# Optimization experiments

Hardware: AMD Instinct MI355X
Metric: run time of the kernel (lower is better)

Reference implementation:

```python
import jax, jax.numpy as jnp
import numpy as np

B, P, C = 8, 16384, 5          # images, proposals/img, classes (incl. background)
K = 100                         # detections_per_img (greedy-NMS iterations)
SCORE_THRESH = 0.05
NMS_THRESH = 0.5
W_XY, W_WH = 10.0, 5.0          # bbox_reg_weights (10,10,5,5)
BBOX_XFORM_CLIP = float(np.log(1000.0 / 16.0))
NEG = jnp.float32(-1e30)


def setup_inputs() -> dict:
    key = jax.random.key(0)
    ks = jax.random.split(key, 8)
    N = B * P
    class_logits = jax.random.normal(ks[0], (N, C), jnp.float32)
    box_regression = jax.random.normal(ks[1], (N, C * 4), jnp.float32) * 0.1
    handside_logits = jax.random.normal(ks[2], (N, C), jnp.float32)
    dxdymag_logits = jax.random.normal(ks[3], (N, C * 3), jnp.float32)
    contact_logits = jax.random.normal(ks[4], (N, C * 5), jnp.float32)
    # valid proposal boxes x1<x2, y1<y2 inside an ~800x1216 image
    x1 = jax.random.uniform(ks[5], (B, P), jnp.float32) * 1100.0
    y1 = jax.random.uniform(ks[6], (B, P), jnp.float32) * 700.0
    wh = jax.random.uniform(ks[7], (B, P, 2), jnp.float32) * 100.0 + 4.0
    proposals = jnp.stack([x1, y1, x1 + wh[..., 0], y1 + wh[..., 1]], axis=-1)
    image_hw = jnp.array([800, 1216], jnp.int32)
    return dict(class_logits=class_logits, box_regression=box_regression,
                handside_logits=handside_logits, dxdymag_logits=dxdymag_logits,
                contact_logits=contact_logits, proposals=proposals, image_hw=image_hw)


def _decode(rel, props):
    # rel [N,C,4], props [N,4] -> [N,C,4] (torchvision BoxCoder.decode)
    w = props[:, 2] - props[:, 0]
    h = props[:, 3] - props[:, 1]
    cx = props[:, 0] + 0.5 * w
    cy = props[:, 1] + 0.5 * h
    dx = rel[..., 0] / W_XY
    dy = rel[..., 1] / W_XY
    dw = jnp.minimum(rel[..., 2] / W_WH, BBOX_XFORM_CLIP)
    dh = jnp.minimum(rel[..., 3] / W_WH, BBOX_XFORM_CLIP)
    pcx = dx * w[:, None] + cx[:, None]
    pcy = dy * h[:, None] + cy[:, None]
    pw = jnp.exp(dw) * w[:, None]
    ph = jnp.exp(dh) * h[:, None]
    return jnp.stack([pcx - 0.5 * pw, pcy - 0.5 * ph,
                      pcx + 0.5 * pw, pcy + 0.5 * ph], axis=-1)


def _iou_one_vs_all(box, boxes):
    lt = jnp.maximum(box[:2], boxes[:, :2])
    rb = jnp.minimum(box[2:], boxes[:, 2:])
    whd = jnp.clip(rb - lt, 0.0)
    inter = whd[:, 0] * whd[:, 1]
    a1 = (box[2] - box[0]) * (box[3] - box[1])
    a2 = (boxes[:, 2] - boxes[:, 0]) * (boxes[:, 3] - boxes[:, 1])
    return inter / (a1 + a2 - inter)


def _nms_image(boxes, scores, labels):
    # class-aware greedy NMS (batched_nms coordinate-offset trick), fixed K iters.
    off = labels.astype(boxes.dtype) * (jax.lax.stop_gradient(boxes).max() + 1.0)
    obox = jax.lax.stop_gradient(boxes) + off[:, None]

    def step(s, _):
        i = jnp.argmax(s)
        keep = s[i] > NEG * 0.5
        iou = _iou_one_vs_all(obox[i], obox)
        s = jnp.where((iou > NMS_THRESH) & keep, NEG, s)
        s = s.at[i].set(NEG)
        return s, (i, keep)

    _, (idx, keep) = jax.lax.scan(step, scores, None, length=K)
    return idx, keep


def reference(class_logits, box_regression, handside_logits, dxdymag_logits,
              contact_logits, proposals, image_hw):
    N = class_logits.shape[0]
    pred_boxes = _decode(box_regression.reshape(N, C, 4), proposals.reshape(-1, 4))
    pred_scores = jax.nn.softmax(class_logits, axis=-1)          # [N,C]
    pred_sides = (jax.nn.sigmoid(handside_logits) > 0.5).astype(jnp.float32)
    pred_dxdy = dxdymag_logits.reshape(N, C, 3)
    pred_contacts = jnp.argmax(contact_logits.reshape(N, C, 5), axis=2)
    # clip boxes to image (image_shape = (H, W))
    Hh = image_hw[0].astype(jnp.float32)
    Ww = image_hw[1].astype(jnp.float32)
    xs = jnp.clip(pred_boxes[..., 0::2], 0.0, Ww)
    ys = jnp.clip(pred_boxes[..., 1::2], 0.0, Hh)
    pred_boxes = jnp.stack([xs[..., 0], ys[..., 0], xs[..., 1], ys[..., 1]], -1)
    # drop background class, flatten per image (class-fastest order, as torch reshape)
    Cm1 = C - 1
    boxes = pred_boxes[:, 1:].reshape(B, P * Cm1, 4)
    scores = pred_scores[:, 1:].reshape(B, P * Cm1)
    sides = pred_sides[:, 1:].reshape(B, P * Cm1)
    dxdy = pred_dxdy[:, 1:].reshape(B, P * Cm1, 3)
    contacts = pred_contacts[:, 1:].reshape(B, P * Cm1)
    labels = jnp.broadcast_to(jnp.tile(jnp.arange(1, C), P), (B, P * Cm1))
    # score thresholding via masking (scores <= thresh never selected)
    ms = jnp.where(scores > SCORE_THRESH, scores, NEG)
    idx, keep = jax.vmap(_nms_image)(boxes, ms, labels)          # [B,K]
    kf = keep.astype(jnp.float32)
    out_boxes = jnp.take_along_axis(boxes, idx[:, :, None], 1) * kf[:, :, None]
    out_scores = jnp.take_along_axis(scores, idx, 1) * kf
    out_labels = jnp.where(keep, jnp.take_along_axis(labels, idx, 1), 0)
    out_sides = jnp.take_along_axis(sides, idx, 1) * kf
    out_dxdy = jnp.take_along_axis(dxdy, idx[:, :, None], 1) * kf[:, :, None]
    out_contacts = jnp.where(keep, jnp.take_along_axis(contacts, idx, 1), 0)
    return (out_boxes, out_scores, out_labels, out_sides, out_dxdy, out_contacts, keep)
```

## Files before the change

### kernel.cpp

```cpp
#include <hip/hip_runtime.h>
#include <cstdint>

typedef unsigned int u32;
typedef unsigned long long u64;

constexpr int B_ = 8;
constexpr int P_ = 16384;
constexpr int K_ = 100;
constexpr int M_ = P_ * 4;
constexpr int TSEL = 192;
constexpr int CAP = 256;
constexpr int NBP = 576;
constexpr u32 BASE16 = 0x3D4Cu;
constexpr float SCORE_T = 0.05f;
constexpr float CLIPV = 4.135166556742356f;


__device__ inline int aphys(int i) {
  return (i < CAP) ? ((((i & 63) + ((i >> 6) << 2)) & 63) | (i & 192)) : i;
}

__device__ inline float4 decode_clip(float4 rel, float4 pr, float Wf, float Hf) {
  const float w  = pr.z - pr.x;
  const float h  = pr.w - pr.y;
  const float cx = pr.x + 0.5f * w;
  const float cy = pr.y + 0.5f * h;
  const float dx = rel.x / 10.0f;
  const float dy = rel.y / 10.0f;
  const float dw = fminf(rel.z / 5.0f, CLIPV);
  const float dh = fminf(rel.w / 5.0f, CLIPV);
  const float pcx = dx * w + cx;
  const float pcy = dy * h + cy;
  const float pw = expf(dw) * w;
  const float ph = expf(dh) * h;
  float x1 = pcx - 0.5f * pw, y1 = pcy - 0.5f * ph;
  float x2 = pcx + 0.5f * pw, y2 = pcy + 0.5f * ph;
  x1 = fminf(fmaxf(x1, 0.f), Wf);
  x2 = fminf(fmaxf(x2, 0.f), Wf);
  y1 = fminf(fmaxf(y1, 0.f), Hf);
  y2 = fminf(fmaxf(y2, 0.f), Hf);
  return make_float4(x1, y1, x2, y2);
}

__global__ __launch_bounds__(256) void prep_kernel(
    const float* __restrict__ logits, const float* __restrict__ boxreg,
    const float* __restrict__ props, const int* __restrict__ image_hw,
    float* __restrict__ wscores, float* __restrict__ wblockmax,
    u32* __restrict__ bhist)
{
  __shared__ u32 lh[NBP];
  __shared__ float red[256];
  for (int i = threadIdx.x; i < NBP; i += 256) lh[i] = 0u;
  __syncthreads();

  const int n = blockIdx.x * 256 + threadIdx.x;

  float l[5];
#pragma unroll
  for (int i = 0; i < 5; ++i) l[i] = logits[n * 5 + i];
  float mx = l[0];
#pragma unroll
  for (int i = 1; i < 5; ++i) mx = fmaxf(mx, l[i]);
  float e[5]; float ssum = 0.f;
#pragma unroll
  for (int i = 0; i < 5; ++i) { e[i] = expf(l[i] - mx); ssum += e[i]; }

  const float4 pr = reinterpret_cast<const float4*>(props)[n];
  const float Hf = (float)image_hw[0];
  const float Wf = (float)image_hw[1];

  float bmax = 0.f;
  float sc[4];
#pragma unroll
  for (int c = 1; c < 5; ++c) {
    const float4 rel = reinterpret_cast<const float4*>(boxreg)[n * 5 + c];
    const float4 bx = decode_clip(rel, pr, Wf, Hf);
    bmax = fmaxf(bmax, fmaxf(fmaxf(bx.x, bx.z), fmaxf(bx.y, bx.w)));
    const float sv = e[c] / ssum;
    sc[c - 1] = sv;
    if (sv > SCORE_T) {
      u32 bin = (__float_as_uint(sv) >> 16) - BASE16;
      if (bin >= (u32)NBP) bin = NBP - 1;
      atomicAdd(&lh[bin], 1u);
    }
  }
  reinterpret_cast<float4*>(wscores)[n] = make_float4(sc[0], sc[1], sc[2], sc[3]);

  __syncthreads();
  for (int i = threadIdx.x; i < NBP; i += 256)
    bhist[(size_t)blockIdx.x * NBP + i] = lh[i];

  red[threadIdx.x] = bmax;
  __syncthreads();
#pragma unroll
  for (int off = 128; off > 0; off >>= 1) {
    if (threadIdx.x < off) red[threadIdx.x] = fmaxf(red[threadIdx.x], red[threadIdx.x + off]);
    __syncthreads();
  }
  if (threadIdx.x == 0) wblockmax[blockIdx.x] = red[0];
}

__global__ __launch_bounds__(64) void thresh_kernel(
    const u32* __restrict__ bhist, u32* __restrict__ Xthr, int* __restrict__ Carr,
    int* __restrict__ remv, int* __restrict__ offs)
{
  const int b = blockIdx.x, t = threadIdx.x;
  const u32* base = bhist + (size_t)(b * 64) * NBP;
  const int lo = NBP - t * 9 - 9;

  u32 hb[9] = {0, 0, 0, 0, 0, 0, 0, 0, 0};
  for (int g = 0; g < 64; ++g) {
    const u32* hg = base + g * NBP + lo;
#pragma unroll
    for (int q = 0; q < 9; ++q) hb[q] += hg[q];
  }
  int mysum = 0;
#pragma unroll
  for (int q = 0; q < 9; ++q) mysum += (int)hb[q];

  int inc = mysum;
#pragma unroll
  for (int off = 1; off < 64; off <<= 1) {
    const int v = __shfl_up(inc, off);
    if (t >= off) inc += v;
  }
  const int tot = __shfl(inc, 63);
  const int pre = inc - mysum;

  int Xi = 0, Cv = 0, remV = 0, binXv = 0;
  if (tot < TSEL) {
    if (t == 63) { Xi = (int)(BASE16 << 16); Cv = tot; remV = 0; binXv = 0; }
  } else if (pre < TSEL && inc >= TSEL) {
    int cum = pre, kb = lo, qsel = 8;
    for (int q = 8; q >= 0; --q) {
      cum += (int)hb[q];
      if (cum >= TSEL) { kb = lo + q; qsel = q; break; }
    }
    int C = cum;
    int Xbin;
    if (C > CAP) { C -= (int)hb[qsel]; Xbin = kb + 1; }
    else Xbin = kb;
    Xi = (int)((BASE16 + (u32)Xbin) << 16);
    Cv = C; remV = tot - C; binXv = Xbin;
  }
#pragma unroll
  for (int off = 32; off > 0; off >>= 1) {
    Xi    = max(Xi,    __shfl_xor(Xi, off));
    Cv    = max(Cv,    __shfl_xor(Cv, off));
    remV  = max(remV,  __shfl_xor(remV, off));
    binXv = max(binXv, __shfl_xor(binXv, off));
  }

  int cg = 0;
  {
    const u32* hg = base + (size_t)t * NBP;
    for (int bin = binXv; bin < NBP; ++bin) cg += (int)hg[bin];
  }
  int inc2 = cg;
#pragma unroll
  for (int off = 1; off < 64; off <<= 1) {
    const int v = __shfl_up(inc2, off);
    if (t >= off) inc2 += v;
  }
  offs[b * 64 + t] = inc2 - cg;
  if (t == 0) { Xthr[b] = (u32)Xi; Carr[b] = Cv; remv[b] = remV; }
}

__global__ __launch_bounds__(256) void compact_kernel(
    const float* __restrict__ wscores, const u32* __restrict__ Xthr,
    const int* __restrict__ offs, u64* __restrict__ keybuf)
{
  const int blk = blockIdx.x;
  const int b = blk >> 6;
  const int n = blk * 256 + threadIdx.x;
  const u32 X = Xthr[b];
  __shared__ int cnt;
  if (threadIdx.x == 0) cnt = 0;
  __syncthreads();
  const int base = b * CAP + offs[blk];

  const float4 v = reinterpret_cast<const float4*>(wscores)[n];
  const float ss[4] = {v.x, v.y, v.z, v.w};
  const int j0 = (n & (P_ - 1)) * 4;
#pragma unroll
  for (int c = 0; c < 4; ++c) {
    if (ss[c] > SCORE_T) {
      const u32 bb = __float_as_uint(ss[c]);
      if (bb >= X) {
        const int pos = atomicAdd(&cnt, 1);
        keybuf[base + pos] = ((u64)bb << 16) | (u64)(65535 - (j0 + c));
      }
    }
  }
}

__global__ __launch_bounds__(512) void nms_kernel(
    const float* __restrict__ boxreg, const float* __restrict__ props,
    const int* __restrict__ image_hw,
    const float* __restrict__ wscores, const float* __restrict__ wblockmax,
    const u32* __restrict__ Xthr, const int* __restrict__ remv,
    const int* __restrict__ Carr, const u64* __restrict__ keybuf,
    const float* __restrict__ handside, const float* __restrict__ dxdymag,
    const float* __restrict__ contact, float* __restrict__ out)
{
  const int b = blockIdx.x, t = threadIdx.x;
  const float4* sc4 = reinterpret_cast<const float4*>(wscores) + (size_t)b * (M_ / 4);
  const u32 X = Xthr[b];
  const float Hf = (float)image_hw[0];
  const float Wf = (float)image_hw[1];

  __shared__ float maxv_s;
  __shared__ u64   kall[CAP];
  __shared__ u64   skey[CAP];
  __shared__ float4 cb4[CAP + K_];
  __shared__ float4 cbx[CAP + K_];
  __shared__ float carea[CAP + K_];
  __shared__ float cscf[CAP + K_];
  __shared__ int   cj[CAP + K_];
  __shared__ u64   supmask[CAP * 4];
  __shared__ int   kidx[K_];
  __shared__ int   kcount_s, nslow_s;
  __shared__ u64   red2[512];
  __shared__ u64   bitmap[1024];

  if (t < 64) {
    float v = wblockmax[b * 64 + t];
#pragma unroll
    for (int off = 32; off > 0; off >>= 1) v = fmaxf(v, __shfl_xor(v, off));
    if (t == 0) maxv_s = v;
  }
  if (t == 0) { kcount_s = 0; nslow_s = 0; }
  const int C = min(Carr[b], CAP);
  if (t < CAP) kall[t] = (t < C) ? keybuf[b * CAP + t] : 0ull;
  __syncthreads();
  const float maxv1 = maxv_s + 1.0f;

  if (t < CAP) {
    const u64 my = kall[t];
    u32 r = 0;
    for (int u = 0; u < CAP; ++u) r += (kall[u] > my) ? 1u : 0u;
    if (t < C) skey[r] = my;
  }
  __syncthreads();

  if (t < C) {
    const u64 key = skey[t];
    const int j = 65535 - (int)(key & 0xFFFFull);
    const int cls = (j & 3) + 1;
    const int n = b * P_ + (j >> 2);
    const float4 rel = reinterpret_cast<const float4*>(boxreg)[n * 5 + cls];
    const float4 pr  = reinterpret_cast<const float4*>(props)[n];
    const float4 bx = decode_clip(rel, pr, Wf, Hf);
    const float offv = (float)cls * maxv1;
    const float ox1 = bx.x + offv, oy1 = bx.y + offv;
    const float ox2 = bx.z + offv, oy2 = bx.w + offv;
    const int ph = aphys(t);
    cb4[ph] = make_float4(ox1, oy1, ox2, oy2);
    cbx[ph] = bx;
    carea[ph] = (ox2 - ox1) * (oy2 - oy1);
    cscf[ph] = __uint_as_float((u32)(key >> 16));
    cj[ph] = j;
  }
  __syncthreads();

  for (int task = t; task < C * 4; task += 512) {
    const int i = task >> 2, wq = task & 3;
    const float4 ib = cb4[aphys(i)];
    const float ia = carea[aphys(i)];
    u64 m = 0;
    const int qb = wq * 64, qe = min(qb + 64, C);
    for (int q = qb; q < qe; ++q) {
      if (q == i) continue;
      const int qp = aphys(q);
      const float4 qbx = cb4[qp];
      const float ltx = fmaxf(ib.x, qbx.x);
      const float lty = fmaxf(ib.y, qbx.y);
      const float rbx = fminf(ib.z, qbx.z);
      const float rby = fminf(ib.w, qbx.w);
      const float iw = fmaxf(rbx - ltx, 0.f);
      const float ih = fmaxf(rby - lty, 0.f);
      const float inter = iw * ih;
      const float iou = inter / (ia + carea[qp] - inter);
      if (iou > 0.5f) m |= 1ull << (q - qb);
    }
    supmask[i * 4 + wq] = m;
  }
  __syncthreads();

  if (t < 64) {
    const u64 lowm = t ? (~0ull >> (64 - t)) : 0ull;
    u64 rb[4][4];
    bool alv[4];
#pragma unroll
    for (int q = 0; q < 4; ++q) {
      const int r = q * 64 + t;
      alv[q] = (r < C);
#pragma unroll
      for (int w = 0; w < 4; ++w) {
        u64 m = supmask[r * 4 + w];
        if (w == q) m &= lowm;
        else if (w > q) m = 0ull;
        rb[q][w] = m;
      }
    }
    u64 km0 = __ballot(alv[0]);
    u64 km1 = __ballot(alv[1]);
    u64 km2 = __ballot(alv[2]);
    u64 km3 = __ballot(alv[3]);
    for (int round = 0; round <= CAP; ++round) {
      const bool k0 = alv[0] && !((rb[0][0] & km0) | (rb[0][1] & km1) | (rb[0][2] & km2) | (rb[0][3] & km3));
      const bool k1 = alv[1] && !((rb[1][0] & km0) | (rb[1][1] & km1) | (rb[1][2] & km2) | (rb[1][3] & km3));
      const bool k2 = alv[2] && !((rb[2][0] & km0) | (rb[2][1] & km1) | (rb[2][2] & km2) | (rb[2][3] & km3));
      const bool k3 = alv[3] && !((rb[3][0] & km0) | (rb[3][1] & km1) | (rb[3][2] & km2) | (rb[3][3] & km3));
      const u64 n0 = __ballot(k0);
      const u64 n1 = __ballot(k1);
      const u64 n2 = __ballot(k2);
      const u64 n3 = __ballot(k3);
      if (n0 == km0 && n1 == km1 && n2 == km2 && n3 == km3) break;
      km0 = n0; km1 = n1; km2 = n2; km3 = n3;
    }
#pragma unroll
    for (int q = 0; q < 4; ++q) {
      const u64 kmq = (q == 0) ? km0 : (q == 1) ? km1 : (q == 2) ? km2 : km3;
      if ((kmq >> t) & 1ull) {
        int rank = __popcll(kmq & lowm);
        if (q > 0) rank += __popcll(km0);
        if (q > 1) rank += __popcll(km1);
        if (q > 2) rank += __popcll(km2);
        if (rank < K_) kidx[rank] = q * 64 + t;
      }
    }
    if (t == 0) {
      kcount_s = min(__popcll(km0) + __popcll(km1) +
                     __popcll(km2) + __popcll(km3), K_);
    }
  }
  __syncthreads();

  if (kcount_s < K_ && remv[b] > 0) {
    for (int i = t; i < 1024; i += 512) bitmap[i] = 0ull;
    __syncthreads();
    while (true) {
      u64 best = 0ull;
      for (int i = t; i < M_ / 4; i += 512) {
        const float4 v = sc4[i];
        const float ss[4] = {v.x, v.y, v.z, v.w};
#pragma unroll
        for (int c = 0; c < 4; ++c) {
          if (ss[c] > SCORE_T) {
            const u32 bb = __float_as_uint(ss[c]);
            if (bb < X) {
              const int j = i * 4 + c;
              if (!((bitmap[j >> 6] >> (j & 63)) & 1ull)) {
                const u64 key = ((u64)bb << 16) | (u64)(65535 - j);
                if (key > best) best = key;
              }
            }
          }
        }
      }
      red2[t] = best;
      __syncthreads();
      for (int off = 256; off > 0; off >>= 1) {
        if (t < off && red2[t + off] > red2[t]) red2[t] = red2[t + off];
        __syncthreads();
      }
      const u64 wkey = red2[0];
      if (wkey == 0ull) break;
      if (t == 0) {
        const int j = 65535 - (int)(wkey & 0xFFFFull);
        bitmap[j >> 6] |= 1ull << (j & 63);
        const int cls = (j & 3) + 1;
        const int n = b * P_ + (j >> 2);
        const float4 rel = reinterpret_cast<const float4*>(boxreg)[n * 5 + cls];
        const float4 pr  = reinterpret_cast<const float4*>(props)[n];
        const float4 bx = decode_clip(rel, pr, Wf, Hf);
        const float offv = (float)cls * maxv1;
        const float ox1 = bx.x + offv, oy1 = bx.y + offv;
        const float ox2 = bx.z + offv, oy2 = bx.w + offv;
        const float ar = (ox2 - ox1) * (oy2 - oy1);
        bool sup = false;
        for (int k2 = 0; k2 < kcount_s; ++k2) {
          const int ki = aphys(kidx[k2]);
          const float4 kb = cb4[ki];
          const float ltx = fmaxf(kb.x, ox1);
          const float lty = fmaxf(kb.y, oy1);
          const float rbx = fminf(kb.z, ox2);
          const float rby = fminf(kb.w, oy2);
          const float iw = fmaxf(rbx - ltx, 0.f);
          const float ih = fmaxf(rby - lty, 0.f);
          const float inter = iw * ih;
          const float iou = inter / (carea[ki] + ar - inter);
          if (iou > 0.5f) { sup = true; break; }
        }
        if (!sup) {
          const int slot = CAP + nslow_s;
          cb4[slot] = make_float4(ox1, oy1, ox2, oy2);
          cbx[slot] = bx;
          carea[slot] = ar;
          cscf[slot] = __uint_as_float((u32)(wkey >> 16));
          cj[slot] = j;
          kidx[kcount_s] = slot;
          ++nslow_s;
          ++kcount_s;
        }
      }
      __syncthreads();
      if (kcount_s >= K_) break;
    }
    __syncthreads();
  }
  __syncthreads();

  const int kc = kcount_s;
  if (t < K_) {
    const int r = t;
    float ob0 = 0.f, ob1 = 0.f, ob2 = 0.f, ob3 = 0.f;
    float osc = 0.f, olab = 0.f, oside = 0.f;
    float od0 = 0.f, od1 = 0.f, od2 = 0.f;
    float ocon = 0.f, okeep = 0.f;
    if (r < kc) {
      const int idx = kidx[r];
      const int ph = aphys(idx);
      const int j = cj[ph];
      const int cls = (j & 3) + 1;
      const int n = b * P_ + (j >> 2);
      const float4 bx = cbx[ph];
      ob0 = bx.x; ob1 = bx.y; ob2 = bx.z; ob3 = bx.w;
      osc = cscf[ph];
      olab = (float)cls;
      oside = (handside[n * 5 + cls] > 0.f) ? 1.f : 0.f;
      od0 = dxdymag[n * 15 + cls * 3 + 0];
      od1 = dxdymag[n * 15 + cls * 3 + 1];
      od2 = dxdymag[n * 15 + cls * 3 + 2];
      float bvv = contact[n * 25 + cls * 5 + 0];
      int best = 0;
#pragma unroll
      for (int i = 1; i < 5; ++i) {
        const float ci = contact[n * 25 + cls * 5 + i];
        if (ci > bvv) { bvv = ci; best = i; }
      }
      ocon = (float)best;
      okeep = 1.f;
    }
    const int gb = b * K_ + r;
    out[gb * 4 + 0] = ob0;
    out[gb * 4 + 1] = ob1;
    out[gb * 4 + 2] = ob2;
    out[gb * 4 + 3] = ob3;
    out[3200 + gb] = osc;
    out[4000 + gb] = olab;
    out[4800 + gb] = oside;
    out[5600 + gb * 3 + 0] = od0;
    out[5600 + gb * 3 + 1] = od1;
    out[5600 + gb * 3 + 2] = od2;
    out[8000 + gb] = ocon;
    out[8800 + gb] = okeep;
  }
}

extern "C" void kernel_launch(void* const* d_in, const int* in_sizes, int n_in,
                              void* d_out, int out_size, void* d_ws, size_t ws_size,
                              hipStream_t stream) {
  const float* class_logits = (const float*)d_in[0];
  const float* box_reg      = (const float*)d_in[1];
  const float* handside     = (const float*)d_in[2];
  const float* dxdymag      = (const float*)d_in[3];
  const float* contact      = (const float*)d_in[4];
  const float* proposals    = (const float*)d_in[5];
  const int*   image_hw     = (const int*)d_in[6];
  float* out = (float*)d_out;

  char* ws = (char*)d_ws;
  u32*   bhist     = (u32*)  ws;
  u32*   Xthr      = (u32*)  (ws + 1179648);
  int*   Carr      = (int*)  (ws + 1179680);
  int*   remv      = (int*)  (ws + 1179712);
  int*   offs      = (int*)  (ws + 1179776);
  float* wblockmax = (float*)(ws + 1181824);
  u64*   keybuf    = (u64*)  (ws + 1183872);
  float* wscores   = (float*)(ws + 2097152);

  prep_kernel<<<dim3(512), dim3(256), 0, stream>>>(
      class_logits, box_reg, proposals, image_hw, wscores, wblockmax, bhist);
  thresh_kernel<<<dim3(B_), dim3(64), 0, stream>>>(
      bhist, Xthr, Carr, remv, offs);
  compact_kernel<<<dim3(512), dim3(256), 0, stream>>>(
      wscores, Xthr, offs, keybuf);
  nms_kernel<<<dim3(B_), dim3(512), 0, stream>>>(
      box_reg, proposals, image_hw, wscores, wblockmax, Xthr, remv, Carr,
      keybuf, handside, dxdymag, contact, out);
}
```

Baseline: 54.73 us.

## Parallelize histogram aggregation and defer per-block offsets to NMS kernel

Replaces the 8-block serial thresh kernel with a 72-block aggregation kernel that sums per-block histograms in parallel. The threshold scan moves into compact_kernel (each block recomputes it) and into nms_kernel. Per-block compaction offsets are now computed in nms_kernel from block counts, and keys are written to per-block slots. The NMS kernel also drops from 512 to 256 threads, which makes the fallback greedy scan serial per thread over twice as many elements and risks extra time whenever that path runs.

```diff
diff --git a/kernel.cpp b/kernel.cpp
--- a/kernel.cpp
+++ b/kernel.cpp
@@ -42,6 +42,45 @@
   return make_float4(x1, y1, x2, y2);
 }
 
+__device__ inline void wave_thresh(const u32* __restrict__ h, int t,
+                                   u32& X, int& Ch, int& rem) {
+  const int lo = NBP - t * 9 - 9;
+  u32 hb[9]; int mysum = 0;
+#pragma unroll
+  for (int q = 0; q < 9; ++q) { hb[q] = h[lo + q]; mysum += (int)hb[q]; }
+  int inc = mysum;
+#pragma unroll
+  for (int off = 1; off < 64; off <<= 1) {
+    const int v = __shfl_up(inc, off);
+    if (t >= off) inc += v;
+  }
+  const int tot = __shfl(inc, 63);
+  const int pre = inc - mysum;
+  int Xi = 0, Cv = 0, remV = 0;
+  if (tot < TSEL) {
+    if (t == 63) { Xi = (int)(BASE16 << 16); Cv = tot; remV = 0; }
+  } else if (pre < TSEL && inc >= TSEL) {
+    int cum = pre, kb = lo, qsel = 8;
+    for (int q = 8; q >= 0; --q) {
+      cum += (int)hb[q];
+      if (cum >= TSEL) { kb = lo + q; qsel = q; break; }
+    }
+    int C = cum;
+    int Xbin;
+    if (C > CAP) { C -= (int)hb[qsel]; Xbin = kb + 1; }
+    else Xbin = kb;
+    Xi = (int)((BASE16 + (u32)Xbin) << 16);
+    Cv = C; remV = tot - C;
+  }
+#pragma unroll
+  for (int off = 32; off > 0; off >>= 1) {
+    Xi   = max(Xi,   __shfl_xor(Xi, off));
+    Cv   = max(Cv,   __shfl_xor(Cv, off));
+    remV = max(remV, __shfl_xor(remV, off));
+  }
+  X = (u32)Xi; Ch = Cv; rem = remV;
+}
+
 __global__ __launch_bounds__(256) void prep_kernel(
     const float* __restrict__ logits, const float* __restrict__ boxreg,
     const float* __restrict__ props, const int* __restrict__ image_hw,
@@ -100,85 +139,39 @@
   if (threadIdx.x == 0) wblockmax[blockIdx.x] = red[0];
 }
 
-__global__ __launch_bounds__(64) void thresh_kernel(
-    const u32* __restrict__ bhist, u32* __restrict__ Xthr, int* __restrict__ Carr,
-    int* __restrict__ remv, int* __restrict__ offs)
+__global__ __launch_bounds__(256) void agg_kernel(
+    const u32* __restrict__ bhist, u32* __restrict__ ahist)
 {
-  const int b = blockIdx.x, t = threadIdx.x;
-  const u32* base = bhist + (size_t)(b * 64) * NBP;
-  const int lo = NBP - t * 9 - 9;
-
-  u32 hb[9] = {0, 0, 0, 0, 0, 0, 0, 0, 0};
-  for (int g = 0; g < 64; ++g) {
-    const u32* hg = base + g * NBP + lo;
-#pragma unroll
-    for (int q = 0; q < 9; ++q) hb[q] += hg[q];
-  }
-  int mysum = 0;
-#pragma unroll
-  for (int q = 0; q < 9; ++q) mysum += (int)hb[q];
-
-  int inc = mysum;
-#pragma unroll
-  for (int off = 1; off < 64; off <<= 1) {
-    const int v = __shfl_up(inc, off);
-    if (t >= off) inc += v;
-  }
-  const int tot = __shfl(inc, 63);
-  const int pre = inc - mysum;
-
-  int Xi = 0, Cv = 0, remV = 0, binXv = 0;
-  if (tot < TSEL) {
-    if (t == 63) { Xi = (int)(BASE16 << 16); Cv = tot; remV = 0; binXv = 0; }
-  } else if (pre < TSEL && inc >= TSEL) {
-    int cum = pre, kb = lo, qsel = 8;
-    for (int q = 8; q >= 0; --q) {
-      cum += (int)hb[q];
-      if (cum >= TSEL) { kb = lo + q; qsel = q; break; }
-    }
-    int C = cum;
-    int Xbin;
-    if (C > CAP) { C -= (int)hb[qsel]; Xbin = kb + 1; }
-    else Xbin = kb;
-    Xi = (int)((BASE16 + (u32)Xbin) << 16);
-    Cv = C; remV = tot - C; binXv = Xbin;
-  }
-#pragma unroll
-  for (int off = 32; off > 0; off >>= 1) {
-    Xi    = max(Xi,    __shfl_xor(Xi, off));
-    Cv    = max(Cv,    __shfl_xor(Cv, off));
-    remV  = max(remV,  __shfl_xor(remV, off));
-    binXv = max(binXv, __shfl_xor(binXv, off));
-  }
-
-  int cg = 0;
-  {
-    const u32* hg = base + (size_t)t * NBP;
-    for (int bin = binXv; bin < NBP; ++bin) cg += (int)hg[bin];
-  }
-  int inc2 = cg;
-#pragma unroll
-  for (int off = 1; off < 64; off <<= 1) {
-    const int v = __shfl_up(inc2, off);
-    if (t >= off) inc2 += v;
-  }
-  offs[b * 64 + t] = inc2 - cg;
-  if (t == 0) { Xthr[b] = (u32)Xi; Carr[b] = Cv; remv[b] = remV; }
+  const int i = blockIdx.x / 9, bb = blockIdx.x % 9;
+  const int lane = threadIdx.x & 63, q = threadIdx.x >> 6;
+  const int bin = bb * 64 + lane;
+  const u32* base = bhist + (size_t)(i * 64) * NBP + bin;
+  u32 s = 0;
+  for (int g = q * 16; g < q * 16 + 16; ++g) s += base[(size_t)g * NBP];
+  __shared__ u32 part[4][64];
+  part[q][lane] = s;
+  __syncthreads();
+  if (q == 0)
+    ahist[i * NBP + bin] = part[0][lane] + part[1][lane] + part[2][lane] + part[3][lane];
 }
 
 __global__ __launch_bounds__(256) void compact_kernel(
-    const float* __restrict__ wscores, const u32* __restrict__ Xthr,
-    const int* __restrict__ offs, u64* __restrict__ keybuf)
+    const float* __restrict__ wscores, const u32* __restrict__ ahist,
+    u64* __restrict__ keybuf2, int* __restrict__ bcnt)
 {
-  const int blk = blockIdx.x;
-  const int b = blk >> 6;
-  const int n = blk * 256 + threadIdx.x;
-  const u32 X = Xthr[b];
+  const int blk = blockIdx.x, b = blk >> 6, t = threadIdx.x;
+  __shared__ u32 Xs;
   __shared__ int cnt;
-  if (threadIdx.x == 0) cnt = 0;
-  __syncthreads();
-  const int base = b * CAP + offs[blk];
-
+  if (t == 0) cnt = 0;
+  if (t < 64) {
+    u32 X; int Ch, rem;
+    wave_thresh(ahist + b * NBP, t, X, Ch, rem);
+    if (t == 0) Xs = X;
+  }
+  __syncthreads();
+  const u32 X = Xs;
+
+  const int n = blk * 256 + t;
   const float4 v = reinterpret_cast<const float4*>(wscores)[n];
   const float ss[4] = {v.x, v.y, v.z, v.w};
   const int j0 = (n & (P_ - 1)) * 4;
@@ -188,28 +181,32 @@
       const u32 bb = __float_as_uint(ss[c]);
       if (bb >= X) {
         const int pos = atomicAdd(&cnt, 1);
-        keybuf[base + pos] = ((u64)bb << 16) | (u64)(65535 - (j0 + c));
-      }
-    }
-  }
-}
-
-__global__ __launch_bounds__(512) void nms_kernel(
+        keybuf2[(size_t)blk * CAP + pos] = ((u64)bb << 16) | (u64)(65535 - (j0 + c));
+      }
+    }
+  }
+  __syncthreads();
+  if (t == 0) bcnt[blk] = cnt;
+}
+
+__global__ __launch_bounds__(256) void nms_kernel(
     const float* __restrict__ boxreg, const float* __restrict__ props,
     const int* __restrict__ image_hw,
     const float* __restrict__ wscores, const float* __restrict__ wblockmax,
-    const u32* __restrict__ Xthr, const int* __restrict__ remv,
-    const int* __restrict__ Carr, const u64* __restrict__ keybuf,
+    const u32* __restrict__ ahist, const int* __restrict__ bcnt,
+    const u64* __restrict__ keybuf2,
     const float* __restrict__ handside, const float* __restrict__ dxdymag,
     const float* __restrict__ contact, float* __restrict__ out)
 {
   const int b = blockIdx.x, t = threadIdx.x;
   const float4* sc4 = reinterpret_cast<const float4*>(wscores) + (size_t)b * (M_ / 4);
-  const u32 X = Xthr[b];
   const float Hf = (float)image_hw[0];
   const float Wf = (float)image_hw[1];
 
   __shared__ float maxv_s;
+  __shared__ u32   X_sh;
+  __shared__ int   rem_sh;
+  __shared__ int   offs2[65];
   __shared__ u64   kall[CAP];
   __shared__ u64   skey[CAP];
   __shared__ float4 cb4[CAP + K_];
@@ -220,22 +217,46 @@
   __shared__ u64   supmask[CAP * 4];
   __shared__ int   kidx[K_];
   __shared__ int   kcount_s, nslow_s;
-  __shared__ u64   red2[512];
+  __shared__ u64   red2[256];
   __shared__ u64   bitmap[1024];
 
+  kall[t] = 0ull;
+  if (t == 0) { kcount_s = 0; nslow_s = 0; }
   if (t < 64) {
-    float v = wblockmax[b * 64 + t];
+    u32 X; int Ch, rem;
+    wave_thresh(ahist + b * NBP, t, X, Ch, rem);
+    if (t == 0) { X_sh = X; rem_sh = rem; }
+    const int cg = bcnt[b * 64 + t];
+    int inc = cg;
+#pragma unroll
+    for (int off = 1; off < 64; off <<= 1) {
+      const int v = __shfl_up(inc, off);
+      if (t >= off) inc += v;
+    }
+    offs2[t] = inc - cg;
+    if (t == 63) offs2[64] = inc;
+  } else if (t >= 64 && t < 128) {
+    float v = wblockmax[b * 64 + (t - 64)];
 #pragma unroll
     for (int off = 32; off > 0; off >>= 1) v = fmaxf(v, __shfl_xor(v, off));
-    if (t == 0) maxv_s = v;
-  }
-  if (t == 0) { kcount_s = 0; nslow_s = 0; }
-  const int C = min(Carr[b], CAP);
-  if (t < CAP) kall[t] = (t < C) ? keybuf[b * CAP + t] : 0ull;
-  __syncthreads();
+    if (t == 64) maxv_s = v;
+  }
+  __syncthreads();
+  const u32 X = X_sh;
   const float maxv1 = maxv_s + 1.0f;
-
-  if (t < CAP) {
+  const int C = min(offs2[64], CAP);
+
+  if (t < C) {
+    int lo2 = 0, hi2 = 64;
+    while (hi2 - lo2 > 1) {
+      const int mid = (lo2 + hi2) >> 1;
+      if (offs2[mid] <= t) lo2 = mid; else hi2 = mid;
+    }
+    kall[t] = keybuf2[(size_t)(b * 64 + lo2) * CAP + (t - offs2[lo2])];
+  }
+  __syncthreads();
+
+  {
     const u64 my = kall[t];
     u32 r = 0;
     for (int u = 0; u < CAP; ++u) r += (kall[u] > my) ? 1u : 0u;
@@ -263,7 +284,7 @@
   }
   __syncthreads();
 
-  for (int task = t; task < C * 4; task += 512) {
+  for (int task = t; task < C * 4; task += 256) {
     const int i = task >> 2, wq = task & 3;
     const float4 ib = cb4[aphys(i)];
     const float ia = carea[aphys(i)];
@@ -337,12 +358,12 @@
   }
   __syncthreads();
 
-  if (kcount_s < K_ && remv[b] > 0) {
-    for (int i = t; i < 1024; i += 512) bitmap[i] = 0ull;
+  if (kcount_s < K_ && rem_sh > 0) {
+    for (int i = t; i < 1024; i += 256) bitmap[i] = 0ull;
     __syncthreads();
     while (true) {
       u64 best = 0ull;
-      for (int i = t; i < M_ / 4; i += 512) {
+      for (int i = t; i < M_ / 4; i += 256) {
         const float4 v = sc4[i];
         const float ss[4] = {v.x, v.y, v.z, v.w};
 #pragma unroll
@@ -361,7 +382,7 @@
       }
       red2[t] = best;
       __syncthreads();
-      for (int off = 256; off > 0; off >>= 1) {
+      for (int off = 128; off > 0; off >>= 1) {
         if (t < off && red2[t + off] > red2[t]) red2[t] = red2[t + off];
         __syncthreads();
       }
@@ -473,21 +494,18 @@
 
   char* ws = (char*)d_ws;
   u32*   bhist     = (u32*)  ws;
-  u32*   Xthr      = (u32*)  (ws + 1179648);
-  int*   Carr      = (int*)  (ws + 1179680);
-  int*   remv      = (int*)  (ws + 1179712);
-  int*   offs      = (int*)  (ws + 1179776);
-  float* wblockmax = (float*)(ws + 1181824);
-  u64*   keybuf    = (u64*)  (ws + 1183872);
-  float* wscores   = (float*)(ws + 2097152);
+  u32*   ahist     = (u32*)  (ws + 1179648);
+  int*   bcnt      = (int*)  (ws + 1198080);
+  float* wblockmax = (float*)(ws + 1200128);
+  u64*   keybuf2   = (u64*)  (ws + 1202176);
+  float* wscores   = (float*)(ws + 2359296);
 
   prep_kernel<<<dim3(512), dim3(256), 0, stream>>>(
       class_logits, box_reg, proposals, image_hw, wscores, wblockmax, bhist);
-  thresh_kernel<<<dim3(B_), dim3(64), 0, stream>>>(
-      bhist, Xthr, Carr, remv, offs);
+  agg_kernel<<<dim3(72), dim3(256), 0, stream>>>(bhist, ahist);
   compact_kernel<<<dim3(512), dim3(256), 0, stream>>>(
-      wscores, Xthr, offs, keybuf);
-  nms_kernel<<<dim3(B_), dim3(512), 0, stream>>>(
-      box_reg, proposals, image_hw, wscores, wblockmax, Xthr, remv, Carr,
-      keybuf, handside, dxdymag, contact, out);
-}
+      wscores, ahist, keybuf2, bcnt);
+  nms_kernel<<<dim3(B_), dim3(256), 0, stream>>>(
+      box_reg, proposals, image_hw, wscores, wblockmax, ahist, bcnt, keybuf2,
+      handside, dxdymag, contact, out);
+}
```

New measurement: 66.06 us. +20.7%, slower.
